# Kernel optimization log

Hardware: AMD Instinct MI355X
Metric: run time of the kernel (lower is better)

Reference implementation:

```python
import jax, jax.numpy as jnp
import numpy as np

LEAKY_ALPHA = 0.2  # tf.nn.leaky_relu default

B, N, D = 4096, 10000, 256

def setup_inputs() -> dict:
    key = jax.random.key(0)
    k1, k2, k3 = jax.random.split(key, 3)
    patient_features = jax.random.normal(k1, (B, D), dtype=jnp.float32)
    disease_nodes = jax.random.normal(k2, (N, D), dtype=jnp.float32) * 0.1
    attn_kernel = jax.random.normal(k3, (2 * D, 1), dtype=jnp.float32) * 0.05
    return {"patient_features": patient_features,
            "disease_nodes": disease_nodes,
            "attn_kernel": attn_kernel}

def reference(patient_features, disease_nodes, attn_kernel):
    # concat([patient, nodes]) @ attn_kernel == patient @ Wp + nodes @ Wn
    d = patient_features.shape[-1]
    Wp = attn_kernel[:d, 0]   # [D]
    Wn = attn_kernel[d:, 0]   # [D]
    score_p = patient_features @ Wp          # [B]
    score_n = disease_nodes @ Wn             # [N]
    scores = score_p[:, None] + score_n[None, :]      # [B, N]
    scores = jnp.where(scores >= 0, scores, LEAKY_ALPHA * scores)
    attn = jax.nn.softmax(scores, axis=1)              # softmax over nodes
    agg = jnp.einsum('bn,nd->bd', attn, disease_nodes)  # weighted sum of nodes
    return patient_features + agg
```

## Files before the change

kernel.cpp:

```cpp
#include <hip/hip_runtime.h>
#include <math.h>

#define NB 4096
#define NN 10000
#define ND 256
#define ALPHA 0.2f
#define CS 16
#define NG (NN / CS)
#define SCHUNK 25
#define NSUPER (NG / SCHUNK)
#define MSEGS 26
#define SEGLEN ((NN + MSEGS - 1) / MSEGS)
#define ZELEMS (NN + 2 * NSUPER * ND + 2 * NSUPER)

typedef unsigned long long u64;

__global__ __launch_bounds__(256) void k_dot(
    const float* __restrict__ P, const float* __restrict__ V,
    const float* __restrict__ K,
    float* __restrict__ t, float* __restrict__ s, u64* __restrict__ tk,
    int* __restrict__ zero_region) {
  int gt = blockIdx.x * 256 + threadIdx.x;
  if (gt < ZELEMS) zero_region[gt] = 0;
  int j = blockIdx.x * 4 + (threadIdx.x >> 6);
  int lane = threadIdx.x & 63;
  if (j >= NN + NB) return;
  const float* row; const float* wv; int oi; bool isn;
  if (j < NN) { row = V + (size_t)j * ND; wv = K + ND; oi = j; isn = true; }
  else        { row = P + (size_t)(j - NN) * ND; wv = K; oi = j - NN; isn = false; }
  float4 r  = ((const float4*)row)[lane];
  float4 kx = ((const float4*)wv)[lane];
  float acc = r.x * kx.x + r.y * kx.y + r.z * kx.z + r.w * kx.w;
  #pragma unroll
  for (int off = 32; off; off >>= 1) acc += __shfl_down(acc, off, 64);
  if (lane == 0) {
    if (isn) {
      t[oi] = acc;
      unsigned bits = __float_as_uint(acc);
      unsigned key = bits ^ (((int)bits >> 31) | 0x80000000u);
      tk[oi] = ((u64)key << 14) | (unsigned)oi;
    } else {
      s[oi] = acc;
    }
  }
}

__global__ __launch_bounds__(256) void k_rank(
    const u64* __restrict__ tk, int* __restrict__ rank) {
  int n = blockIdx.x * 256 + threadIdx.x;
  u64 kn = (n < NN) ? tk[n] : ~0ull;
  int m0 = blockIdx.y * SEGLEN;
  int m1 = min(NN, m0 + SEGLEN);
  int r = 0;
  int m = m0;
  #pragma unroll 1
  for (; m + 4 <= m1; m += 4) {
    u64 a = tk[m], b2 = tk[m + 1], c = tk[m + 2], dd = tk[m + 3];
    r += (a < kn) + (b2 < kn) + (c < kn) + (dd < kn);
  }
  for (; m < m1; ++m) r += (tk[m] < kn);
  if (n < NN && r) atomicAdd(&rank[n], r);
}

__global__ __launch_bounds__(256) void k_scatter(
    const float* __restrict__ t, const int* __restrict__ rank,
    float* __restrict__ tsort, float* __restrict__ eA, float* __restrict__ eC,
    int* __restrict__ idxs) {
  int n = blockIdx.x * 256 + threadIdx.x;
  if (n < NN) {
    int r = rank[n];
    float tn = t[n];
    tsort[r] = tn;
    eA[r] = __expf(tn);
    eC[r] = __expf(ALPHA * tn);
    idxs[r] = n;
  }
}

__global__ __launch_bounds__(256) void k_chunk(
    const float* __restrict__ eA, const float* __restrict__ eC,
    const int* __restrict__ idxs, const float* __restrict__ V,
    const float* __restrict__ s, const float* __restrict__ tsort,
    float* __restrict__ SA, float* __restrict__ SC,
    float* __restrict__ sa0, float* __restrict__ sc0,
    float* __restrict__ SSA, float* __restrict__ SSC,
    float* __restrict__ ssa0, float* __restrict__ ssc0,
    int* __restrict__ kk) {
  int g = blockIdx.x, d = threadIdx.x;
  if (g < NG) {
    int base = g * CS;
    float accA = 0.f, accC = 0.f, sa = 0.f, sc = 0.f;
    #pragma unroll
    for (int j = 0; j < CS; ++j) {
      int i = base + j;
      float ea = eA[i], ec = eC[i];
      float v = V[(size_t)idxs[i] * ND + d];
      accA += ea * v; accC += ec * v;
      sa += ea; sc += ec;
    }
    SA[(size_t)g * ND + d] = accA;
    SC[(size_t)g * ND + d] = accC;
    int gs = g / SCHUNK;
    atomicAdd(&SSA[(size_t)gs * ND + d], accA);
    atomicAdd(&SSC[(size_t)gs * ND + d], accC);
    if (d == 0) {
      sa0[g] = sa; sc0[g] = sc;
      atomicAdd(&ssa0[gs], sa);
      atomicAdd(&ssc0[gs], sc);
    }
  } else {
    int b = (g - NG) * 256 + d;
    float key = -s[b];
    int lo = 0, hi = NN;
    while (lo < hi) {
      int mid = (lo + hi) >> 1;
      if (tsort[mid] < key) lo = mid + 1; else hi = mid;
    }
    kk[b] = lo;
  }
}

__global__ __launch_bounds__(256) void k_finalize(
    const float* __restrict__ P, const float* __restrict__ V,
    const float* __restrict__ s, const int* __restrict__ kk,
    const float* __restrict__ eA, const float* __restrict__ eC,
    const int* __restrict__ idxs,
    const float* __restrict__ SA, const float* __restrict__ SC,
    const float* __restrict__ sa0, const float* __restrict__ sc0,
    const float* __restrict__ SSA, const float* __restrict__ SSC,
    const float* __restrict__ ssa0, const float* __restrict__ ssc0,
    float* __restrict__ out) {
  int b = blockIdx.x, d = threadIdx.x;
  int k = kk[b];
  int g = k >> 4;
  int gs = g / SCHUNK;
  float suffA = 0.f, prefC = 0.f, suffa = 0.f, prefc = 0.f;
  for (int q = gs; q < NSUPER; ++q) {
    suffA += SSA[(size_t)q * ND + d];
    suffa += ssa0[q];
  }
  for (int q = 0; q < gs; ++q) {
    prefC += SSC[(size_t)q * ND + d];
    prefc += ssc0[q];
  }
  for (int j = gs * SCHUNK; j < g; ++j) {
    suffA -= SA[(size_t)j * ND + d];
    prefC += SC[(size_t)j * ND + d];
    suffa -= sa0[j];
    prefc += sc0[j];
  }
  for (int i = g << 4; i < k; ++i) {
    float ea = eA[i], ec = eC[i];
    float v = V[(size_t)idxs[i] * ND + d];
    suffA -= ea * v; prefC += ec * v;
    suffa -= ea;     prefc += ec;
  }
  float sb = s[b];
  float ea = __expf(sb), ec = __expf(ALPHA * sb);
  float l = ea * suffa + ec * prefc;
  float agg = (ea * suffA + ec * prefC) / l;
  out[(size_t)b * ND + d] = P[(size_t)b * ND + d] + agg;
}

extern "C" void kernel_launch(void* const* d_in, const int* in_sizes, int n_in,
                              void* d_out, int out_size, void* d_ws, size_t ws_size,
                              hipStream_t stream) {
  const float* P = (const float*)d_in[0];
  const float* V = (const float*)d_in[1];
  const float* K = (const float*)d_in[2];
  float* out = (float*)d_out;

  char* w = (char*)d_ws;
  u64*   tk    = (u64*)w;   w += sizeof(u64) * NN;
  int*   zreg  = (int*)w;
  int*   rank  = (int*)w;   w += sizeof(int) * NN;
  float* SSA   = (float*)w; w += sizeof(float) * NSUPER * ND;
  float* SSC   = (float*)w; w += sizeof(float) * NSUPER * ND;
  float* ssa0  = (float*)w; w += sizeof(float) * NSUPER;
  float* ssc0  = (float*)w; w += sizeof(float) * NSUPER;
  float* t     = (float*)w; w += sizeof(float) * NN;
  float* s     = (float*)w; w += sizeof(float) * NB;
  float* tsort = (float*)w; w += sizeof(float) * NN;
  float* eA    = (float*)w; w += sizeof(float) * NN;
  float* eC    = (float*)w; w += sizeof(float) * NN;
  int*   idxs  = (int*)w;   w += sizeof(int) * NN;
  int*   kk    = (int*)w;   w += sizeof(int) * NB;
  float* SA    = (float*)w; w += sizeof(float) * (size_t)NG * ND;
  float* SC    = (float*)w; w += sizeof(float) * (size_t)NG * ND;
  float* sa0   = (float*)w; w += sizeof(float) * NG;
  float* sc0   = (float*)w; w += sizeof(float) * NG;

  k_dot<<<(NN + NB + 3) / 4, 256, 0, stream>>>(P, V, K, t, s, tk, zreg);
  k_rank<<<dim3((NN + 255) / 256, MSEGS), 256, 0, stream>>>(tk, rank);
  k_scatter<<<(NN + 255) / 256, 256, 0, stream>>>(t, rank, tsort, eA, eC, idxs);
  k_chunk<<<NG + NB / 256, 256, 0, stream>>>(eA, eC, idxs, V, s, tsort,
                                             SA, SC, sa0, sc0,
                                             SSA, SSC, ssa0, ssc0, kk);
  k_finalize<<<NB, 256, 0, stream>>>(P, V, s, kk, eA, eC, idxs,
                                     SA, SC, sa0, sc0, SSA, SSC, ssa0, ssc0, out);
}
```

Before: 127.2 us.

## Fuse five phase kernels into one cooperative persistent kernel with grid syncs

Merges the dot, rank, scatter, chunk and finalize kernels into a single cooperative kernel of 1024 persistent blocks that loops over work and uses grid-wide barriers between phases. This removes four kernel launch boundaries and their launch gaps. It falls back to launching each phase as a separate kernel if occupancy is too low. The trade-offs are grid-sync cost, fixed grid-stride work distribution (finalize now loops four rows per block), and the rank segment count changing from 26 to 25.

```diff
diff --git a/kernel.cpp b/kernel.cpp
--- a/kernel.cpp
+++ b/kernel.cpp
@@ -1,5 +1,8 @@
 #include <hip/hip_runtime.h>
+#include <hip/hip_cooperative_groups.h>
 #include <math.h>
+
+namespace cg = cooperative_groups;
 
 #define NB 4096
 #define NN 10000
@@ -9,193 +12,220 @@
 #define NG (NN / CS)
 #define SCHUNK 25
 #define NSUPER (NG / SCHUNK)
-#define MSEGS 26
-#define SEGLEN ((NN + MSEGS - 1) / MSEGS)
+#define MSEGS 25
+#define SEGLEN (NN / MSEGS)
 #define ZELEMS (NN + 2 * NSUPER * ND + 2 * NSUPER)
+#define GRID 1024
 
 typedef unsigned long long u64;
 
-__global__ __launch_bounds__(256) void k_dot(
-    const float* __restrict__ P, const float* __restrict__ V,
-    const float* __restrict__ K,
-    float* __restrict__ t, float* __restrict__ s, u64* __restrict__ tk,
-    int* __restrict__ zero_region) {
-  int gt = blockIdx.x * 256 + threadIdx.x;
-  if (gt < ZELEMS) zero_region[gt] = 0;
-  int j = blockIdx.x * 4 + (threadIdx.x >> 6);
-  int lane = threadIdx.x & 63;
-  if (j >= NN + NB) return;
-  const float* row; const float* wv; int oi; bool isn;
-  if (j < NN) { row = V + (size_t)j * ND; wv = K + ND; oi = j; isn = true; }
-  else        { row = P + (size_t)(j - NN) * ND; wv = K; oi = j - NN; isn = false; }
-  float4 r  = ((const float4*)row)[lane];
-  float4 kx = ((const float4*)wv)[lane];
-  float acc = r.x * kx.x + r.y * kx.y + r.z * kx.z + r.w * kx.w;
-  #pragma unroll
-  for (int off = 32; off; off >>= 1) acc += __shfl_down(acc, off, 64);
-  if (lane == 0) {
-    if (isn) {
-      t[oi] = acc;
-      unsigned bits = __float_as_uint(acc);
-      unsigned key = bits ^ (((int)bits >> 31) | 0x80000000u);
-      tk[oi] = ((u64)key << 14) | (unsigned)oi;
+struct Args {
+  const float *P, *V, *K;
+  float *out;
+  u64 *tk;
+  int *zreg, *rank;
+  float *SSA, *SSC, *ssa0, *ssc0;
+  float *t, *s, *tsort, *eA, *eC;
+  int *idxs, *kk;
+  float *SA, *SC, *sa0, *sc0;
+};
+
+__device__ __forceinline__ void phaseA(const Args& a, int bid, int tid, int nblk) {
+  int gtid = bid * 256 + tid;
+  int nth = nblk * 256;
+  for (int i = gtid; i < ZELEMS; i += nth) a.zreg[i] = 0;
+  int lane = tid & 63;
+  int wv = bid * 4 + (tid >> 6);
+  for (int j = wv; j < NN + NB; j += nblk * 4) {
+    bool isn = (j < NN);
+    const float* row = isn ? a.V + (size_t)j * ND : a.P + (size_t)(j - NN) * ND;
+    const float* wgt = isn ? a.K + ND : a.K;
+    float4 r  = ((const float4*)row)[lane];
+    float4 kx = ((const float4*)wgt)[lane];
+    float acc = r.x * kx.x + r.y * kx.y + r.z * kx.z + r.w * kx.w;
+    #pragma unroll
+    for (int off = 32; off; off >>= 1) acc += __shfl_down(acc, off, 64);
+    if (lane == 0) {
+      if (isn) {
+        a.t[j] = acc;
+        unsigned bits = __float_as_uint(acc);
+        unsigned key = bits ^ (((int)bits >> 31) | 0x80000000u);
+        a.tk[j] = ((u64)key << 14) | (unsigned)j;
+      } else {
+        a.s[j - NN] = acc;
+      }
+    }
+  }
+}
+
+__device__ __forceinline__ void phaseB(const Args& a, int bid, int tid, int nblk) {
+  for (int tb = bid; tb < MSEGS * 40; tb += nblk) {
+    int seg = tb / 40;
+    int n = (tb % 40) * 256 + tid;
+    u64 kn = (n < NN) ? a.tk[n] : ~0ull;
+    int m0 = seg * SEGLEN;
+    int m1 = m0 + SEGLEN;
+    int r = 0;
+    #pragma unroll 1
+    for (int m = m0; m < m1; m += 4) {
+      u64 x0 = a.tk[m], x1 = a.tk[m + 1], x2 = a.tk[m + 2], x3 = a.tk[m + 3];
+      r += (x0 < kn) + (x1 < kn) + (x2 < kn) + (x3 < kn);
+    }
+    if (n < NN && r) atomicAdd(&a.rank[n], r);
+  }
+}
+
+__device__ __forceinline__ void phaseC(const Args& a, int bid, int tid, int nblk) {
+  int nth = nblk * 256;
+  for (int n = bid * 256 + tid; n < NN; n += nth) {
+    int r = a.rank[n];
+    float tn = a.t[n];
+    a.tsort[r] = tn;
+    a.eA[r] = __expf(tn);
+    a.eC[r] = __expf(ALPHA * tn);
+    a.idxs[r] = n;
+  }
+}
+
+__device__ __forceinline__ void phaseD(const Args& a, int bid, int tid, int nblk) {
+  for (int g = bid; g < NG + NB / 256; g += nblk) {
+    if (g < NG) {
+      int base = g * CS, d = tid;
+      float accA = 0.f, accC = 0.f, sa = 0.f, sc = 0.f;
+      #pragma unroll
+      for (int jj = 0; jj < CS; ++jj) {
+        int i = base + jj;
+        float ea = a.eA[i], ec = a.eC[i];
+        float v = a.V[(size_t)a.idxs[i] * ND + d];
+        accA += ea * v; accC += ec * v;
+        sa += ea; sc += ec;
+      }
+      a.SA[(size_t)g * ND + d] = accA;
+      a.SC[(size_t)g * ND + d] = accC;
+      int gs = g / SCHUNK;
+      atomicAdd(&a.SSA[(size_t)gs * ND + d], accA);
+      atomicAdd(&a.SSC[(size_t)gs * ND + d], accC);
+      if (d == 0) {
+        a.sa0[g] = sa; a.sc0[g] = sc;
+        atomicAdd(&a.ssa0[gs], sa);
+        atomicAdd(&a.ssc0[gs], sc);
+      }
     } else {
-      s[oi] = acc;
-    }
-  }
-}
-
-__global__ __launch_bounds__(256) void k_rank(
-    const u64* __restrict__ tk, int* __restrict__ rank) {
-  int n = blockIdx.x * 256 + threadIdx.x;
-  u64 kn = (n < NN) ? tk[n] : ~0ull;
-  int m0 = blockIdx.y * SEGLEN;
-  int m1 = min(NN, m0 + SEGLEN);
-  int r = 0;
-  int m = m0;
-  #pragma unroll 1
-  for (; m + 4 <= m1; m += 4) {
-    u64 a = tk[m], b2 = tk[m + 1], c = tk[m + 2], dd = tk[m + 3];
-    r += (a < kn) + (b2 < kn) + (c < kn) + (dd < kn);
-  }
-  for (; m < m1; ++m) r += (tk[m] < kn);
-  if (n < NN && r) atomicAdd(&rank[n], r);
-}
-
-__global__ __launch_bounds__(256) void k_scatter(
-    const float* __restrict__ t, const int* __restrict__ rank,
-    float* __restrict__ tsort, float* __restrict__ eA, float* __restrict__ eC,
-    int* __restrict__ idxs) {
-  int n = blockIdx.x * 256 + threadIdx.x;
-  if (n < NN) {
-    int r = rank[n];
-    float tn = t[n];
-    tsort[r] = tn;
-    eA[r] = __expf(tn);
-    eC[r] = __expf(ALPHA * tn);
-    idxs[r] = n;
-  }
-}
-
-__global__ __launch_bounds__(256) void k_chunk(
-    const float* __restrict__ eA, const float* __restrict__ eC,
-    const int* __restrict__ idxs, const float* __restrict__ V,
-    const float* __restrict__ s, const float* __restrict__ tsort,
-    float* __restrict__ SA, float* __restrict__ SC,
-    float* __restrict__ sa0, float* __restrict__ sc0,
-    float* __restrict__ SSA, float* __restrict__ SSC,
-    float* __restrict__ ssa0, float* __restrict__ ssc0,
-    int* __restrict__ kk) {
-  int g = blockIdx.x, d = threadIdx.x;
-  if (g < NG) {
-    int base = g * CS;
-    float accA = 0.f, accC = 0.f, sa = 0.f, sc = 0.f;
-    #pragma unroll
-    for (int j = 0; j < CS; ++j) {
-      int i = base + j;
-      float ea = eA[i], ec = eC[i];
-      float v = V[(size_t)idxs[i] * ND + d];
-      accA += ea * v; accC += ec * v;
-      sa += ea; sc += ec;
-    }
-    SA[(size_t)g * ND + d] = accA;
-    SC[(size_t)g * ND + d] = accC;
+      int b = (g - NG) * 256 + tid;
+      float key = -a.s[b];
+      int lo = 0, hi = NN;
+      while (lo < hi) {
+        int mid = (lo + hi) >> 1;
+        if (a.tsort[mid] < key) lo = mid + 1; else hi = mid;
+      }
+      a.kk[b] = lo;
+    }
+  }
+}
+
+__device__ __forceinline__ void phaseE(const Args& a, int bid, int tid, int nblk) {
+  for (int b = bid; b < NB; b += nblk) {
+    int d = tid;
+    int k = a.kk[b];
+    int g = k >> 4;
     int gs = g / SCHUNK;
-    atomicAdd(&SSA[(size_t)gs * ND + d], accA);
-    atomicAdd(&SSC[(size_t)gs * ND + d], accC);
-    if (d == 0) {
-      sa0[g] = sa; sc0[g] = sc;
-      atomicAdd(&ssa0[gs], sa);
-      atomicAdd(&ssc0[gs], sc);
-    }
-  } else {
-    int b = (g - NG) * 256 + d;
-    float key = -s[b];
-    int lo = 0, hi = NN;
-    while (lo < hi) {
-      int mid = (lo + hi) >> 1;
-      if (tsort[mid] < key) lo = mid + 1; else hi = mid;
-    }
-    kk[b] = lo;
-  }
-}
-
-__global__ __launch_bounds__(256) void k_finalize(
-    const float* __restrict__ P, const float* __restrict__ V,
-    const float* __restrict__ s, const int* __restrict__ kk,
-    const float* __restrict__ eA, const float* __restrict__ eC,
-    const int* __restrict__ idxs,
-    const float* __restrict__ SA, const float* __restrict__ SC,
-    const float* __restrict__ sa0, const float* __restrict__ sc0,
-    const float* __restrict__ SSA, const float* __restrict__ SSC,
-    const float* __restrict__ ssa0, const float* __restrict__ ssc0,
-    float* __restrict__ out) {
-  int b = blockIdx.x, d = threadIdx.x;
-  int k = kk[b];
-  int g = k >> 4;
-  int gs = g / SCHUNK;
-  float suffA = 0.f, prefC = 0.f, suffa = 0.f, prefc = 0.f;
-  for (int q = gs; q < NSUPER; ++q) {
-    suffA += SSA[(size_t)q * ND + d];
-    suffa += ssa0[q];
-  }
-  for (int q = 0; q < gs; ++q) {
-    prefC += SSC[(size_t)q * ND + d];
-    prefc += ssc0[q];
-  }
-  for (int j = gs * SCHUNK; j < g; ++j) {
-    suffA -= SA[(size_t)j * ND + d];
-    prefC += SC[(size_t)j * ND + d];
-    suffa -= sa0[j];
-    prefc += sc0[j];
-  }
-  for (int i = g << 4; i < k; ++i) {
-    float ea = eA[i], ec = eC[i];
-    float v = V[(size_t)idxs[i] * ND + d];
-    suffA -= ea * v; prefC += ec * v;
-    suffa -= ea;     prefc += ec;
-  }
-  float sb = s[b];
-  float ea = __expf(sb), ec = __expf(ALPHA * sb);
-  float l = ea * suffa + ec * prefc;
-  float agg = (ea * suffA + ec * prefC) / l;
-  out[(size_t)b * ND + d] = P[(size_t)b * ND + d] + agg;
+    float suffA = 0.f, prefC = 0.f, suffa = 0.f, prefc = 0.f;
+    for (int q = gs; q < NSUPER; ++q) {
+      suffA += a.SSA[(size_t)q * ND + d];
+      suffa += a.ssa0[q];
+    }
+    for (int q = 0; q < gs; ++q) {
+      prefC += a.SSC[(size_t)q * ND + d];
+      prefc += a.ssc0[q];
+    }
+    for (int j = gs * SCHUNK; j < g; ++j) {
+      suffA -= a.SA[(size_t)j * ND + d];
+      prefC += a.SC[(size_t)j * ND + d];
+      suffa -= a.sa0[j];
+      prefc += a.sc0[j];
+    }
+    for (int i = g << 4; i < k; ++i) {
+      float ea = a.eA[i], ec = a.eC[i];
+      float v = a.V[(size_t)a.idxs[i] * ND + d];
+      suffA -= ea * v; prefC += ec * v;
+      suffa -= ea;     prefc += ec;
+    }
+    float sb = a.s[b];
+    float ea = __expf(sb), ec = __expf(ALPHA * sb);
+    float l = ea * suffa + ec * prefc;
+    float agg = (ea * suffA + ec * prefC) / l;
+    a.out[(size_t)b * ND + d] = a.P[(size_t)b * ND + d] + agg;
+  }
+}
+
+__global__ __launch_bounds__(256, 4) void fused_all(Args a) {
+  cg::grid_group gg = cg::this_grid();
+  int tid = threadIdx.x, bid = blockIdx.x, nblk = gridDim.x;
+  phaseA(a, bid, tid, nblk);
+  gg.sync();
+  phaseB(a, bid, tid, nblk);
+  gg.sync();
+  phaseC(a, bid, tid, nblk);
+  gg.sync();
+  phaseD(a, bid, tid, nblk);
+  gg.sync();
+  phaseE(a, bid, tid, nblk);
+}
+
+__global__ __launch_bounds__(256, 4) void fused_one(Args a, int ph) {
+  int tid = threadIdx.x, bid = blockIdx.x, nblk = gridDim.x;
+  switch (ph) {
+    case 0: phaseA(a, bid, tid, nblk); break;
+    case 1: phaseB(a, bid, tid, nblk); break;
+    case 2: phaseC(a, bid, tid, nblk); break;
+    case 3: phaseD(a, bid, tid, nblk); break;
+    case 4: phaseE(a, bid, tid, nblk); break;
+  }
 }
 
 extern "C" void kernel_launch(void* const* d_in, const int* in_sizes, int n_in,
                               void* d_out, int out_size, void* d_ws, size_t ws_size,
                               hipStream_t stream) {
-  const float* P = (const float*)d_in[0];
-  const float* V = (const float*)d_in[1];
-  const float* K = (const float*)d_in[2];
-  float* out = (float*)d_out;
+  Args a;
+  a.P = (const float*)d_in[0];
+  a.V = (const float*)d_in[1];
+  a.K = (const float*)d_in[2];
+  a.out = (float*)d_out;
 
   char* w = (char*)d_ws;
-  u64*   tk    = (u64*)w;   w += sizeof(u64) * NN;
-  int*   zreg  = (int*)w;
-  int*   rank  = (int*)w;   w += sizeof(int) * NN;
-  float* SSA   = (float*)w; w += sizeof(float) * NSUPER * ND;
-  float* SSC   = (float*)w; w += sizeof(float) * NSUPER * ND;
-  float* ssa0  = (float*)w; w += sizeof(float) * NSUPER;
-  float* ssc0  = (float*)w; w += sizeof(float) * NSUPER;
-  float* t     = (float*)w; w += sizeof(float) * NN;
-  float* s     = (float*)w; w += sizeof(float) * NB;
-  float* tsort = (float*)w; w += sizeof(float) * NN;
-  float* eA    = (float*)w; w += sizeof(float) * NN;
-  float* eC    = (float*)w; w += sizeof(float) * NN;
-  int*   idxs  = (int*)w;   w += sizeof(int) * NN;
-  int*   kk    = (int*)w;   w += sizeof(int) * NB;
-  float* SA    = (float*)w; w += sizeof(float) * (size_t)NG * ND;
-  float* SC    = (float*)w; w += sizeof(float) * (size_t)NG * ND;
-  float* sa0   = (float*)w; w += sizeof(float) * NG;
-  float* sc0   = (float*)w; w += sizeof(float) * NG;
-
-  k_dot<<<(NN + NB + 3) / 4, 256, 0, stream>>>(P, V, K, t, s, tk, zreg);
-  k_rank<<<dim3((NN + 255) / 256, MSEGS), 256, 0, stream>>>(tk, rank);
-  k_scatter<<<(NN + 255) / 256, 256, 0, stream>>>(t, rank, tsort, eA, eC, idxs);
-  k_chunk<<<NG + NB / 256, 256, 0, stream>>>(eA, eC, idxs, V, s, tsort,
-                                             SA, SC, sa0, sc0,
-                                             SSA, SSC, ssa0, ssc0, kk);
-  k_finalize<<<NB, 256, 0, stream>>>(P, V, s, kk, eA, eC, idxs,
-                                     SA, SC, sa0, sc0, SSA, SSC, ssa0, ssc0, out);
-}
+  a.tk = (u64*)w;    w += sizeof(u64) * NN;
+  a.zreg = (int*)w;
+  a.rank = (int*)w;  w += sizeof(int) * NN;
+  a.SSA = (float*)w; w += sizeof(float) * NSUPER * ND;
+  a.SSC = (float*)w; w += sizeof(float) * NSUPER * ND;
+  a.ssa0 = (float*)w; w += sizeof(float) * NSUPER;
+  a.ssc0 = (float*)w; w += sizeof(float) * NSUPER;
+  a.t = (float*)w;     w += sizeof(float) * NN;
+  a.s = (float*)w;     w += sizeof(float) * NB;
+  a.tsort = (float*)w; w += sizeof(float) * NN;
+  a.eA = (float*)w;    w += sizeof(float) * NN;
+  a.eC = (float*)w;    w += sizeof(float) * NN;
+  a.idxs = (int*)w;    w += sizeof(int) * NN;
+  a.kk = (int*)w;      w += sizeof(int) * NB;
+  a.SA = (float*)w;    w += sizeof(float) * (size_t)NG * ND;
+  a.SC = (float*)w;    w += sizeof(float) * (size_t)NG * ND;
+  a.sa0 = (float*)w;   w += sizeof(float) * NG;
+  a.sc0 = (float*)w;   w += sizeof(float) * NG;
+
+  static int coop_ok = -1;
+  if (coop_ok < 0) {
+    int nb = 0;
+    if (hipOccupancyMaxActiveBlocksPerMultiprocessor(
+            &nb, (const void*)fused_all, 256, 0) != hipSuccess) nb = 0;
+    coop_ok = (nb >= GRID / 256) ? 1 : 0;
+  }
+
+  if (coop_ok) {
+    void* kargs[] = {(void*)&a};
+    hipLaunchCooperativeKernel((const void*)fused_all, dim3(GRID), dim3(256),
+                               kargs, 0, stream);
+  } else {
+    for (int ph = 0; ph < 5; ++ph)
+      fused_one<<<dim3(GRID), dim3(256), 0, stream>>>(a, ph);
+  }
+}
```

Result: slower. 150.4 us (+18.3%).

## Fuse rank counting and scatter into one kernel with shared-memory reduction

Applied to the files above, without the earlier changes.

Replaces the separate rank kernel (global atomics over 26 segments) and scatter kernel with one kernel. Each block handles 16 nodes across 16 segments, reduces the partial ranks in shared memory and scatters directly. This drops a launch, the rank buffer, its zeroing and the global atomics. In exchange, within a wavefront the 16 lanes of a segment read the same tk addresses while the 4 segments read different addresses, so loads are broadcast-like and not coalesced. Each thread also scans 625 keys serially.

```diff
diff --git a/kernel.cpp b/kernel.cpp
--- a/kernel.cpp
+++ b/kernel.cpp
@@ -9,9 +9,9 @@
 #define NG (NN / CS)
 #define SCHUNK 25
 #define NSUPER (NG / SCHUNK)
-#define MSEGS 26
-#define SEGLEN ((NN + MSEGS - 1) / MSEGS)
-#define ZELEMS (NN + 2 * NSUPER * ND + 2 * NSUPER)
+#define RSEGS 16
+#define RSEGLEN (NN / RSEGS)
+#define ZELEMS (2 * NSUPER * ND + 2 * NSUPER)
 
 typedef unsigned long long u64;
 
@@ -45,35 +45,38 @@
   }
 }
 
-__global__ __launch_bounds__(256) void k_rank(
-    const u64* __restrict__ tk, int* __restrict__ rank) {
-  int n = blockIdx.x * 256 + threadIdx.x;
-  u64 kn = (n < NN) ? tk[n] : ~0ull;
-  int m0 = blockIdx.y * SEGLEN;
-  int m1 = min(NN, m0 + SEGLEN);
+__global__ __launch_bounds__(256) void k_ranksc(
+    const u64* __restrict__ tk, const float* __restrict__ t,
+    float* __restrict__ tsort, float* __restrict__ eA, float* __restrict__ eC,
+    int* __restrict__ idxs) {
+  __shared__ int lr[CS][RSEGS + 1];
+  int g = blockIdx.x;
+  int nl = threadIdx.x & 15;
+  int seg = threadIdx.x >> 4;
+  int n = g * CS + nl;
+  u64 kn = tk[n];
+  int m0 = seg * RSEGLEN;
+  int m1 = m0 + RSEGLEN;
   int r = 0;
   int m = m0;
   #pragma unroll 1
   for (; m + 4 <= m1; m += 4) {
-    u64 a = tk[m], b2 = tk[m + 1], c = tk[m + 2], dd = tk[m + 3];
-    r += (a < kn) + (b2 < kn) + (c < kn) + (dd < kn);
+    u64 a = tk[m], b = tk[m + 1], c = tk[m + 2], d = tk[m + 3];
+    r += (a < kn) + (b < kn) + (c < kn) + (d < kn);
   }
   for (; m < m1; ++m) r += (tk[m] < kn);
-  if (n < NN && r) atomicAdd(&rank[n], r);
-}
-
-__global__ __launch_bounds__(256) void k_scatter(
-    const float* __restrict__ t, const int* __restrict__ rank,
-    float* __restrict__ tsort, float* __restrict__ eA, float* __restrict__ eC,
-    int* __restrict__ idxs) {
-  int n = blockIdx.x * 256 + threadIdx.x;
-  if (n < NN) {
-    int r = rank[n];
-    float tn = t[n];
-    tsort[r] = tn;
-    eA[r] = __expf(tn);
-    eC[r] = __expf(ALPHA * tn);
-    idxs[r] = n;
+  lr[nl][seg] = r;
+  __syncthreads();
+  if (threadIdx.x < CS) {
+    int rr = 0;
+    #pragma unroll
+    for (int q = 0; q < RSEGS; ++q) rr += lr[threadIdx.x][q];
+    int n2 = g * CS + threadIdx.x;
+    float tn = t[n2];
+    tsort[rr] = tn;
+    eA[rr] = __expf(tn);
+    eC[rr] = __expf(ALPHA * tn);
+    idxs[rr] = n2;
   }
 }
 
@@ -173,7 +176,6 @@
   char* w = (char*)d_ws;
   u64*   tk    = (u64*)w;   w += sizeof(u64) * NN;
   int*   zreg  = (int*)w;
-  int*   rank  = (int*)w;   w += sizeof(int) * NN;
   float* SSA   = (float*)w; w += sizeof(float) * NSUPER * ND;
   float* SSC   = (float*)w; w += sizeof(float) * NSUPER * ND;
   float* ssa0  = (float*)w; w += sizeof(float) * NSUPER;
@@ -191,8 +193,7 @@
   float* sc0   = (float*)w; w += sizeof(float) * NG;
 
   k_dot<<<(NN + NB + 3) / 4, 256, 0, stream>>>(P, V, K, t, s, tk, zreg);
-  k_rank<<<dim3((NN + 255) / 256, MSEGS), 256, 0, stream>>>(tk, rank);
-  k_scatter<<<(NN + 255) / 256, 256, 0, stream>>>(t, rank, tsort, eA, eC, idxs);
+  k_ranksc<<<NG, 256, 0, stream>>>(tk, t, tsort, eA, eC, idxs);
   k_chunk<<<NG + NB / 256, 256, 0, stream>>>(eA, eC, idxs, V, s, tsort,
                                              SA, SC, sa0, sc0,
                                              SSA, SSC, ssa0, ssc0, kk);
```

New measurement: 145.4 us. 14.3% more time.
